# Optimization experiments

Hardware: AMD Instinct MI355X
Metric: run time of the kernel (lower is better)

## Reference

```python
import jax, jax.numpy as jnp
import numpy as np

B, Q, K, D, H = 8, 128, 1024, 256, 256


def setup_inputs() -> dict:
    key = jax.random.key(0)
    ks = jax.random.split(key, 7)
    queries = jax.random.normal(ks[0], (B, Q, D), dtype=jnp.float32)
    keys = jax.random.normal(ks[1], (B, K, D), dtype=jnp.float32)
    values = jax.random.normal(ks[2], (B, K, D), dtype=jnp.float32)
    W_q = jax.random.normal(ks[3], (H, D), dtype=jnp.float32) * (1.0 / np.sqrt(D))
    W_k = jax.random.normal(ks[4], (H, D), dtype=jnp.float32) * (1.0 / np.sqrt(D))
    w_v = jax.random.normal(ks[5], (H,), dtype=jnp.float32) * (1.0 / np.sqrt(H))
    valid_lens = jax.random.randint(ks[6], (B,), 0, K, dtype=jnp.int64)
    return {"queries": queries, "keys": keys, "values": values,
            "W_q": W_q, "W_k": W_k, "w_v": w_v, "valid_lens": valid_lens}


def reference(queries, keys, values, W_q, W_k, w_v, valid_lens):
    # Linear projections (bias=False): [B,Q,H], [B,K,H]
    q = jnp.einsum("bqd,hd->bqh", queries, W_q)
    k = jnp.einsum("bkd,hd->bkh", keys, W_k)
    # Broadcast add -> tanh -> reduce with w_v: scores [B,Q,K]
    features = jnp.tanh(q[:, :, None, :] + k[:, None, :, :])  # [B,Q,K,H]
    scores = jnp.einsum("bqkh,h->bqk", features, w_v)
    # Masked softmax over K: positions >= valid_len get -1e9
    mask = jnp.arange(K)[None, None, :] < valid_lens[:, None, None]
    scores = jnp.where(mask, scores, jnp.float32(-1e9))
    attn = jax.nn.softmax(scores, axis=-1)  # [B,Q,K]
    # Dropout p=0.0 (eval): identity. bmm(attn, values) -> [B,Q,Dv]
    return jnp.einsum("bqk,bkv->bqv", attn, values)
```

## Files before the change

### kernel.cpp

```cpp
#include <hip/hip_runtime.h>

#define BB 8
#define QQ 128
#define KK 1024
#define DD 256
#define HH 256

#define KSPLIT 8
#define KCH (KK / KSPLIT)
#define QT 8

#define TWO_LOG2E     2.8853900817779268f
#define NEG_TWO_LOG2E -2.8853900817779268f

__global__ __launch_bounds__(256) void proj_kernel(const float* __restrict__ queries,
                                                   const float* __restrict__ keys,
                                                   const float* __restrict__ Wq,
                                                   const float* __restrict__ Wk,
                                                   float* __restrict__ eproj) {
    __shared__ float As[64][68];
    __shared__ float Ws[64][68];
    const int t  = threadIdx.x;
    const int tr = t & 15;
    const int th = t >> 4;
    const int r0 = blockIdx.x * 64;
    const int h0 = blockIdx.y * 64;
    const bool isQ = (r0 < BB * QQ);
    const float* A = isQ ? (queries + (size_t)r0 * DD)
                         : (keys + (size_t)(r0 - BB * QQ) * DD);
    const float* W = isQ ? Wq : Wk;

    float acc[4][4] = {};

    for (int dc = 0; dc < DD; dc += 64) {
#pragma unroll
        for (int i = 0; i < 4; ++i) {
            int fi  = t + 256 * i;
            int row = fi >> 4;
            int c4  = (fi & 15) << 2;
            *(float4*)&As[row][c4] = *(const float4*)&A[(size_t)row * DD + dc + c4];
            *(float4*)&Ws[row][c4] = *(const float4*)&W[(size_t)(h0 + row) * DD + dc + c4];
        }
        __syncthreads();
#pragma unroll 4
        for (int dd = 0; dd < 64; dd += 4) {
            float4 a4[4], w4[4];
#pragma unroll
            for (int i = 0; i < 4; ++i) a4[i] = *(float4*)&As[tr + 16 * i][dd];
#pragma unroll
            for (int i = 0; i < 4; ++i) w4[i] = *(float4*)&Ws[th + 16 * i][dd];
#pragma unroll
            for (int ri = 0; ri < 4; ++ri)
#pragma unroll
                for (int hi = 0; hi < 4; ++hi) {
                    acc[ri][hi] += a4[ri].x * w4[hi].x + a4[ri].y * w4[hi].y +
                                   a4[ri].z * w4[hi].z + a4[ri].w * w4[hi].w;
                }
        }
        __syncthreads();
    }
#pragma unroll
    for (int ri = 0; ri < 4; ++ri)
#pragma unroll
        for (int hi = 0; hi < 4; ++hi) {
            eproj[(size_t)(r0 + tr + 16 * ri) * HH + h0 + th + 16 * hi] =
                __builtin_amdgcn_exp2f(TWO_LOG2E * acc[ri][hi]);
        }
}

__global__ __launch_bounds__(256) void score_kernel(const float* __restrict__ eproj,
                                                    const float* __restrict__ wv,
                                                    const int* __restrict__ vlen,
                                                    float* __restrict__ p) {
    __shared__ float qs[32][68];
    __shared__ float ks_[32][68];
    __shared__ float ws[64];
    const int t  = threadIdx.x;
    const int tk = t & 15;
    const int tq = t >> 4;
    const int b  = blockIdx.z;
    const int q0 = blockIdx.y * 32;
    const int k0 = blockIdx.x * 32;

    const float* qpB = eproj + ((size_t)(b * QQ + q0)) * HH;
    const float* kpB = eproj + ((size_t)(BB * QQ + b * KK + k0)) * HH;

    float acc[2][2] = {};

    for (int hc = 0; hc < HH; hc += 64) {
#pragma unroll
        for (int i = 0; i < 2; ++i) {
            int fi = t + 256 * i; int row = fi >> 4; int c4 = (fi & 15) << 2;
            *(float4*)&qs[row][c4]  = *(const float4*)&qpB[(size_t)row * HH + hc + c4];
            *(float4*)&ks_[row][c4] = *(const float4*)&kpB[(size_t)row * HH + hc + c4];
        }
        if (t < 16) *(float4*)&ws[t * 4] = *(const float4*)&wv[hc + t * 4];
        __syncthreads();

#pragma unroll 4
        for (int hh = 0; hh < 64; hh += 4) {
            float4 w4 = *(float4*)&ws[hh];
            const float* wa = (const float*)&w4;
            float4 q4[2], k4[2];
            q4[0] = *(float4*)&qs[tq][hh];
            q4[1] = *(float4*)&qs[tq + 16][hh];
            k4[0] = *(float4*)&ks_[tk][hh];
            k4[1] = *(float4*)&ks_[tk + 16][hh];
#pragma unroll
            for (int i = 0; i < 2; ++i) {
                const float* qa = (const float*)&q4[i];
#pragma unroll
                for (int j = 0; j < 2; ++j) {
                    const float* ka = (const float*)&k4[j];
#pragma unroll
                    for (int c = 0; c < 4; ++c) {
                        float d = __builtin_fmaf(qa[c], ka[c], 1.0f);
                        acc[i][j] += wa[c] * __builtin_amdgcn_rcpf(d);
                    }
                }
            }
        }
        __syncthreads();
    }

    const int vl = vlen[b];
#pragma unroll
    for (int i = 0; i < 2; ++i)
#pragma unroll
        for (int j = 0; j < 2; ++j) {
            int q = q0 + tq + 16 * i;
            int k = k0 + tk + 16 * j;
            float pv;
            if (vl == 0) pv = 1.0f;
            else pv = (k < vl) ? __builtin_amdgcn_exp2f(NEG_TWO_LOG2E * acc[i][j])
                               : 0.0f;
            p[((size_t)b * QQ + q) * KK + k] = pv;
        }
}

__global__ __launch_bounds__(256) void av_partial(const float* __restrict__ p,
                                                  const float* __restrict__ V,
                                                  float* __restrict__ partial,
                                                  float* __restrict__ psum) {
    __shared__ float a_s[QT][KCH];
    const int t   = threadIdx.x;
    const int ksb = blockIdx.x;
    const int q0  = blockIdx.y * QT;
    const int b   = blockIdx.z;
    const int kc0 = ksb * KCH;

    const float* pB = p + ((size_t)b * QQ + q0) * KK + kc0;
    const float* VB = V + ((size_t)b * KK + kc0) * DD;

    {
        int qi = t >> 5;
        int k4 = (t & 31) << 2;
        *(float4*)&a_s[qi][k4] = *(const float4*)&pB[(size_t)qi * KK + k4];
    }
    __syncthreads();

    if (t < QT) {
        float s = 0.f;
        for (int x = 0; x < KCH; x += 4) {
            float4 v = *(float4*)&a_s[t][x];
            s += v.x + v.y + v.z + v.w;
        }
        psum[((size_t)ksb * BB + b) * QQ + q0 + t] = s;
    }

    float acc[QT] = {};
    float vc[8], vn[8];
#pragma unroll
    for (int j = 0; j < 8; ++j) vc[j] = VB[(size_t)j * DD + t];

    for (int kg = 0; kg < KCH; kg += 8) {
        if (kg + 8 < KCH) {
#pragma unroll
            for (int j = 0; j < 8; ++j) vn[j] = VB[(size_t)(kg + 8 + j) * DD + t];
        }
#pragma unroll
        for (int qi = 0; qi < QT; ++qi) {
            float4 a0 = *(float4*)&a_s[qi][kg];
            float4 a1 = *(float4*)&a_s[qi][kg + 4];
            acc[qi] += a0.x * vc[0] + a0.y * vc[1] + a0.z * vc[2] + a0.w * vc[3] +
                       a1.x * vc[4] + a1.y * vc[5] + a1.z * vc[6] + a1.w * vc[7];
        }
#pragma unroll
        for (int j = 0; j < 8; ++j) vc[j] = vn[j];
    }

#pragma unroll
    for (int qi = 0; qi < QT; ++qi) {
        partial[(size_t)ksb * (BB * QQ * DD) +
                ((size_t)b * QQ + q0 + qi) * DD + t] = acc[qi];
    }
}

__global__ __launch_bounds__(256) void av_reduce(const float* __restrict__ partial,
                                                 const float* __restrict__ psum,
                                                 float* __restrict__ out) {
    const int i  = blockIdx.x * 256 + threadIdx.x;
    const int bq = i >> 6;

    float S = 0.f;
#pragma unroll
    for (int ks = 0; ks < KSPLIT; ++ks) S += psum[(size_t)ks * (BB * QQ) + bq];

    const float4* p4 = (const float4*)partial;
    const int stride4 = BB * QQ * DD / 4;
    float4 s = p4[i];
#pragma unroll
    for (int ks = 1; ks < KSPLIT; ++ks) {
        float4 x = p4[(size_t)ks * stride4 + i];
        s.x += x.x; s.y += x.y; s.z += x.z; s.w += x.w;
    }
    const float inv = 1.0f / S;
    s.x *= inv; s.y *= inv; s.z *= inv; s.w *= inv;
    ((float4*)out)[i] = s;
}

extern "C" void kernel_launch(void* const* d_in, const int* in_sizes, int n_in,
                              void* d_out, int out_size, void* d_ws, size_t ws_size,
                              hipStream_t stream) {
    const float* queries = (const float*)d_in[0];
    const float* keys    = (const float*)d_in[1];
    const float* values  = (const float*)d_in[2];
    const float* W_q     = (const float*)d_in[3];
    const float* W_k     = (const float*)d_in[4];
    const float* w_v     = (const float*)d_in[5];
    const int*   vlen    = (const int*)d_in[6];
    float* out = (float*)d_out;

    float* ws    = (float*)d_ws;
    float* eproj = ws;
    float* p     = ws + (size_t)(BB * QQ + BB * KK) * HH;
    float* psum  = p + (size_t)BB * QQ * KK;
    float* partial = ws;

    proj_kernel<<<dim3((BB * QQ + BB * KK) / 64, HH / 64, 1), 256, 0, stream>>>(
        queries, keys, W_q, W_k, eproj);

    score_kernel<<<dim3(KK / 32, QQ / 32, BB), 256, 0, stream>>>(eproj, w_v, vlen, p);

    av_partial<<<dim3(KSPLIT, QQ / QT, BB), 256, 0, stream>>>(p, values, partial, psum);

    av_reduce<<<dim3(BB * QQ * DD / 4 / 256, 1, 1), 256, 0, stream>>>(partial, psum, out);
}
```

Before: 156.3 us.

## Enlarge projection and score tiles and double-buffer score kernel shared loads

The projection kernel now computes a 64x128 output tile per block instead of 64x64, and the score kernel computes 32x64 instead of 32x32. Both raise register-level reuse of shared-memory operands. The score kernel also double-buffers its shared tiles, prefetching the next H chunk into registers while computing the current one, which removes one barrier per chunk. In exchange each thread uses more registers, there are fewer blocks, and shared memory per block grows, all of which may lower occupancy.

New measurement: 176.1 us. 12.6% more time.

```diff
diff --git a/kernel.cpp b/kernel.cpp
--- a/kernel.cpp
+++ b/kernel.cpp
@@ -19,40 +19,42 @@
                                                    const float* __restrict__ Wk,
                                                    float* __restrict__ eproj) {
     __shared__ float As[64][68];
-    __shared__ float Ws[64][68];
+    __shared__ float Ws[128][68];
     const int t  = threadIdx.x;
     const int tr = t & 15;
     const int th = t >> 4;
     const int r0 = blockIdx.x * 64;
-    const int h0 = blockIdx.y * 64;
+    const int h0 = blockIdx.y * 128;
     const bool isQ = (r0 < BB * QQ);
     const float* A = isQ ? (queries + (size_t)r0 * DD)
                          : (keys + (size_t)(r0 - BB * QQ) * DD);
     const float* W = isQ ? Wq : Wk;
 
-    float acc[4][4] = {};
+    float acc[4][8] = {};
 
     for (int dc = 0; dc < DD; dc += 64) {
 #pragma unroll
         for (int i = 0; i < 4; ++i) {
-            int fi  = t + 256 * i;
-            int row = fi >> 4;
-            int c4  = (fi & 15) << 2;
+            int fi = t + 256 * i; int row = fi >> 4; int c4 = (fi & 15) << 2;
             *(float4*)&As[row][c4] = *(const float4*)&A[(size_t)row * DD + dc + c4];
+        }
+#pragma unroll
+        for (int i = 0; i < 8; ++i) {
+            int fi = t + 256 * i; int row = fi >> 4; int c4 = (fi & 15) << 2;
             *(float4*)&Ws[row][c4] = *(const float4*)&W[(size_t)(h0 + row) * DD + dc + c4];
         }
         __syncthreads();
-#pragma unroll 4
+#pragma unroll 2
         for (int dd = 0; dd < 64; dd += 4) {
-            float4 a4[4], w4[4];
+            float4 a4[4], w4[8];
 #pragma unroll
             for (int i = 0; i < 4; ++i) a4[i] = *(float4*)&As[tr + 16 * i][dd];
 #pragma unroll
-            for (int i = 0; i < 4; ++i) w4[i] = *(float4*)&Ws[th + 16 * i][dd];
+            for (int j = 0; j < 8; ++j) w4[j] = *(float4*)&Ws[th + 16 * j][dd];
 #pragma unroll
             for (int ri = 0; ri < 4; ++ri)
 #pragma unroll
-                for (int hi = 0; hi < 4; ++hi) {
+                for (int hi = 0; hi < 8; ++hi) {
                     acc[ri][hi] += a4[ri].x * w4[hi].x + a4[ri].y * w4[hi].y +
                                    a4[ri].z * w4[hi].z + a4[ri].w * w4[hi].w;
                 }
@@ -62,7 +64,7 @@
 #pragma unroll
     for (int ri = 0; ri < 4; ++ri)
 #pragma unroll
-        for (int hi = 0; hi < 4; ++hi) {
+        for (int hi = 0; hi < 8; ++hi) {
             eproj[(size_t)(r0 + tr + 16 * ri) * HH + h0 + th + 16 * hi] =
                 __builtin_amdgcn_exp2f(TWO_LOG2E * acc[ri][hi]);
         }
@@ -72,62 +74,98 @@
                                                     const float* __restrict__ wv,
                                                     const int* __restrict__ vlen,
                                                     float* __restrict__ p) {
-    __shared__ float qs[32][68];
-    __shared__ float ks_[32][68];
-    __shared__ float ws[64];
+    __shared__ float qs[2][32][68];
+    __shared__ float ks_[2][64][68];
+    __shared__ float ws[2][64];
     const int t  = threadIdx.x;
     const int tk = t & 15;
     const int tq = t >> 4;
     const int b  = blockIdx.z;
     const int q0 = blockIdx.y * 32;
-    const int k0 = blockIdx.x * 32;
+    const int k0 = blockIdx.x * 64;
 
     const float* qpB = eproj + ((size_t)(b * QQ + q0)) * HH;
     const float* kpB = eproj + ((size_t)(BB * QQ + b * KK + k0)) * HH;
 
-    float acc[2][2] = {};
-
-    for (int hc = 0; hc < HH; hc += 64) {
-#pragma unroll
-        for (int i = 0; i < 2; ++i) {
-            int fi = t + 256 * i; int row = fi >> 4; int c4 = (fi & 15) << 2;
-            *(float4*)&qs[row][c4]  = *(const float4*)&qpB[(size_t)row * HH + hc + c4];
-            *(float4*)&ks_[row][c4] = *(const float4*)&kpB[(size_t)row * HH + hc + c4];
-        }
-        if (t < 16) *(float4*)&ws[t * 4] = *(const float4*)&wv[hc + t * 4];
-        __syncthreads();
-
-#pragma unroll 4
+#pragma unroll
+    for (int i = 0; i < 2; ++i) {
+        int fi = t + 256 * i; int row = fi >> 4; int c4 = (fi & 15) << 2;
+        *(float4*)&qs[0][row][c4] = *(const float4*)&qpB[(size_t)row * HH + c4];
+    }
+#pragma unroll
+    for (int i = 0; i < 4; ++i) {
+        int fi = t + 256 * i; int row = fi >> 4; int c4 = (fi & 15) << 2;
+        *(float4*)&ks_[0][row][c4] = *(const float4*)&kpB[(size_t)row * HH + c4];
+    }
+    if (t < 16) *(float4*)&ws[0][t * 4] = *(const float4*)&wv[t * 4];
+    __syncthreads();
+
+    float acc[2][4] = {};
+
+    for (int c = 0; c < 4; ++c) {
+        const int cur = c & 1, nxt = cur ^ 1;
+
+        float4 pq[2], pk[4], pw;
+        if (c < 3) {
+            const int hc = (c + 1) * 64;
+#pragma unroll
+            for (int i = 0; i < 2; ++i) {
+                int fi = t + 256 * i; int row = fi >> 4; int c4 = (fi & 15) << 2;
+                pq[i] = *(const float4*)&qpB[(size_t)row * HH + hc + c4];
+            }
+#pragma unroll
+            for (int i = 0; i < 4; ++i) {
+                int fi = t + 256 * i; int row = fi >> 4; int c4 = (fi & 15) << 2;
+                pk[i] = *(const float4*)&kpB[(size_t)row * HH + hc + c4];
+            }
+            if (t < 16) pw = *(const float4*)&wv[hc + t * 4];
+        }
+
+#pragma unroll 2
         for (int hh = 0; hh < 64; hh += 4) {
-            float4 w4 = *(float4*)&ws[hh];
+            float4 w4 = *(float4*)&ws[cur][hh];
             const float* wa = (const float*)&w4;
-            float4 q4[2], k4[2];
-            q4[0] = *(float4*)&qs[tq][hh];
-            q4[1] = *(float4*)&qs[tq + 16][hh];
-            k4[0] = *(float4*)&ks_[tk][hh];
-            k4[1] = *(float4*)&ks_[tk + 16][hh];
+            float4 q4[2], k4[4];
+            q4[0] = *(float4*)&qs[cur][tq][hh];
+            q4[1] = *(float4*)&qs[cur][tq + 16][hh];
+#pragma unroll
+            for (int j = 0; j < 4; ++j) k4[j] = *(float4*)&ks_[cur][tk + 16 * j][hh];
 #pragma unroll
             for (int i = 0; i < 2; ++i) {
                 const float* qa = (const float*)&q4[i];
 #pragma unroll
-                for (int j = 0; j < 2; ++j) {
+                for (int j = 0; j < 4; ++j) {
                     const float* ka = (const float*)&k4[j];
 #pragma unroll
-                    for (int c = 0; c < 4; ++c) {
-                        float d = __builtin_fmaf(qa[c], ka[c], 1.0f);
-                        acc[i][j] += wa[c] * __builtin_amdgcn_rcpf(d);
+                    for (int cc = 0; cc < 4; ++cc) {
+                        float d = __builtin_fmaf(qa[cc], ka[cc], 1.0f);
+                        acc[i][j] += wa[cc] * __builtin_amdgcn_rcpf(d);
                     }
                 }
             }
         }
-        __syncthreads();
+
+        if (c < 3) {
+#pragma unroll
+            for (int i = 0; i < 2; ++i) {
+                int fi = t + 256 * i; int row = fi >> 4; int c4 = (fi & 15) << 2;
+                *(float4*)&qs[nxt][row][c4] = pq[i];
+            }
+#pragma unroll
+            for (int i = 0; i < 4; ++i) {
+                int fi = t + 256 * i; int row = fi >> 4; int c4 = (fi & 15) << 2;
+                *(float4*)&ks_[nxt][row][c4] = pk[i];
+            }
+            if (t < 16) *(float4*)&ws[nxt][t * 4] = pw;
+            __syncthreads();
+        }
     }
 
     const int vl = vlen[b];
 #pragma unroll
     for (int i = 0; i < 2; ++i)
 #pragma unroll
-        for (int j = 0; j < 2; ++j) {
+        for (int j = 0; j < 4; ++j) {
             int q = q0 + tq + 16 * i;
             int k = k0 + tk + 16 * j;
             float pv;
@@ -237,10 +275,10 @@
     float* psum  = p + (size_t)BB * QQ * KK;
     float* partial = ws;
 
-    proj_kernel<<<dim3((BB * QQ + BB * KK) / 64, HH / 64, 1), 256, 0, stream>>>(
+    proj_kernel<<<dim3((BB * QQ + BB * KK) / 64, HH / 128, 1), 256, 0, stream>>>(
         queries, keys, W_q, W_k, eproj);
 
-    score_kernel<<<dim3(KK / 32, QQ / 32, BB), 256, 0, stream>>>(eproj, w_v, vlen, p);
+    score_kernel<<<dim3(KK / 64, QQ / 32, BB), 256, 0, stream>>>(eproj, w_v, vlen, p);
 
     av_partial<<<dim3(KSPLIT, QQ / QT, BB), 256, 0, stream>>>(p, values, partial, psum);
 
```
